# Performance work log

Measured on AMD Instinct MI355X. Metric: run time of the kernel, lower is better.

Reference implementation:

```python
import jax, jax.numpy as jnp
import numpy as np

SCALE, Z, X, Y = 4, 9, 9, 9
INV_SQRT_2PI = 1.0 / np.sqrt(2.0 * np.pi)


def setup_inputs() -> dict:
    key = jax.random.key(0)
    k1, = jax.random.split(key, 1)
    inp = jax.random.normal(k1, (1, 1, 128, 512, 512), dtype=jnp.float32)
    return {
        "inp": inp,
        "mu_z": jnp.asarray(0.0, dtype=jnp.float32),
        "sig_z": jnp.asarray(0.1, dtype=jnp.float32),
        "bet_xy": jnp.asarray(2.0, dtype=jnp.float32),
        "bet_z": jnp.asarray(1.5, dtype=jnp.float32),
    }


def _gen_alf(bet_xy, bet_z):
    # squared distances along each axis; torch's loop overwrites the wrap-around
    # write, so the net result for odd sizes is simply (arange - size//2)**2
    zd = ((jnp.arange(Z) - Z // 2) ** 2).astype(jnp.float32)[:, None, None]
    xd = ((jnp.arange(X) - X // 2) ** 2).astype(jnp.float32)[None, :, None]
    yd = ((jnp.arange(Y) - Y // 2) ** 2).astype(jnp.float32)[None, None, :]
    d_2 = zd / bet_z ** 2 + (xd + yd) / bet_xy ** 2  # (Z, X, Y)
    return jnp.exp(-d_2 / 2) * INV_SQRT_2PI


def reference(inp, mu_z, sig_z, bet_xy, bet_z):
    z0 = jnp.exp(mu_z + 0.5 * sig_z ** 2)
    rec = inp * z0  # (N, 1, D, H, W)
    alf = _gen_alf(bet_xy, bet_z)[None, None]  # (1, 1, Z, X, Y)
    pad_z = (Z - SCALE + 1) // 2
    rec = jax.lax.conv_general_dilated(
        rec, alf,
        window_strides=(SCALE, 1, 1),
        padding=[(pad_z, pad_z), (X // 2, X // 2), (Y // 2, Y // 2)],
        dimension_numbers=("NCDHW", "OIDHW", "NCDHW"),
    )  # (N, 1, D//SCALE, H, W)
    rec = (rec - rec.min()) / (rec.max() - rec.min())
    return rec
```

## Files before the change

kernel.cpp:

```cpp
#include <hip/hip_runtime.h>

#define D_IN  128
#define D_OUT 32
#define H     512
#define W     512
#define W4    128
#define HB    16
#define ZR    (HB + 8)
#define NTHR  512

__global__ __launch_bounds__(NTHR)
void conv3d_fused(const float* __restrict__ inp, float* __restrict__ out,
                  const float* __restrict__ bxy_p, const float* __restrict__ bz_p,
                  float* __restrict__ blkMin, float* __restrict__ blkMax) {
    __shared__ float zbuf[ZR * W];
    __shared__ float hbuf[HB * W];

    const int d  = blockIdx.x >> 5;
    const int h0 = (blockIdx.x & 31) * HB;

    const float bz = bz_p[0], bx = bxy_p[0];
    const float iz = 1.0f / (2.0f * bz * bz);
    const float ix = 1.0f / (2.0f * bx * bx);
    float wz[9], wx[9];
#pragma unroll
    for (int k = 0; k < 9; ++k) {
        float dd = (float)(k - 4);
        wz[k] = expf(-dd * dd * iz);
        wx[k] = expf(-dd * dd * ix);
    }

    const float4* in4 = (const float4*)inp;
    float4* z4 = (float4*)zbuf;
    float4* h4 = (float4*)hbuf;

    for (int t = threadIdx.x; t < ZR * W4; t += NTHR) {
        int r  = t >> 7;
        int c4 = t & (W4 - 1);
        int h  = h0 - 4 + r;
        float4 acc = make_float4(0.f, 0.f, 0.f, 0.f);
        if ((unsigned)h < H) {
            int base = h * W4 + c4;
#pragma unroll
            for (int k = 0; k < 9; ++k) {
                int din = 4 * d - 3 + k;
                if ((unsigned)din < D_IN) {
                    float4 v = in4[din * (H * W4) + base];
                    acc.x += v.x * wz[k]; acc.y += v.y * wz[k];
                    acc.z += v.z * wz[k]; acc.w += v.w * wz[k];
                }
            }
        }
        z4[t] = acc;
    }
    __syncthreads();

    for (int t = threadIdx.x; t < HB * W4; t += NTHR) {
        int r  = t >> 7;
        int c4 = t & (W4 - 1);
        float4 acc = make_float4(0.f, 0.f, 0.f, 0.f);
#pragma unroll
        for (int k = 0; k < 9; ++k) {
            float4 v = z4[(r + k) * W4 + c4];
            acc.x += v.x * wx[k]; acc.y += v.y * wx[k];
            acc.z += v.z * wx[k]; acc.w += v.w * wx[k];
        }
        h4[t] = acc;
    }
    __syncthreads();

    float lmin =  3.402823466e38f;
    float lmax = -3.402823466e38f;
    float4* out4 = (float4*)out;
    for (int t = threadIdx.x; t < HB * W4; t += NTHR) {
        int r  = t >> 7;
        int c4 = t & (W4 - 1);
        float4 zv = make_float4(0.f, 0.f, 0.f, 0.f);
        float4 va = (c4 > 0)      ? h4[r * W4 + c4 - 1] : zv;
        float4 vb =                 h4[r * W4 + c4];
        float4 vc = (c4 < W4 - 1) ? h4[r * W4 + c4 + 1] : zv;
        float win[12] = {va.x, va.y, va.z, va.w,
                         vb.x, vb.y, vb.z, vb.w,
                         vc.x, vc.y, vc.z, vc.w};
        float4 o = make_float4(0.f, 0.f, 0.f, 0.f);
#pragma unroll
        for (int k = 0; k < 9; ++k) {
            o.x += win[k]     * wx[k];
            o.y += win[k + 1] * wx[k];
            o.z += win[k + 2] * wx[k];
            o.w += win[k + 3] * wx[k];
        }
        out4[(d * H + h0 + r) * W4 + c4] = o;
        lmin = fminf(lmin, fminf(fminf(o.x, o.y), fminf(o.z, o.w)));
        lmax = fmaxf(lmax, fmaxf(fmaxf(o.x, o.y), fmaxf(o.z, o.w)));
    }

#pragma unroll
    for (int off = 32; off > 0; off >>= 1) {
        lmin = fminf(lmin, __shfl_down(lmin, off, 64));
        lmax = fmaxf(lmax, __shfl_down(lmax, off, 64));
    }
    float* smin = &zbuf[0];
    float* smax = &zbuf[16];
    int lane = threadIdx.x & 63, wv = threadIdx.x >> 6;
    if (lane == 0) { smin[wv] = lmin; smax[wv] = lmax; }
    __syncthreads();
    if (threadIdx.x == 0) {
        float mn = smin[0], mx = smax[0];
#pragma unroll
        for (int i = 1; i < 8; ++i) { mn = fminf(mn, smin[i]); mx = fmaxf(mx, smax[i]); }
        blkMin[blockIdx.x] = mn;
        blkMax[blockIdx.x] = mx;
    }
}

__global__ void reduce_kernel(const float* __restrict__ blkMin, const float* __restrict__ blkMax,
                              float* __restrict__ fin, int nblk) {
    float lmin =  3.402823466e38f;
    float lmax = -3.402823466e38f;
    for (int i = threadIdx.x; i < nblk; i += blockDim.x) {
        lmin = fminf(lmin, blkMin[i]);
        lmax = fmaxf(lmax, blkMax[i]);
    }
#pragma unroll
    for (int off = 32; off > 0; off >>= 1) {
        lmin = fminf(lmin, __shfl_down(lmin, off, 64));
        lmax = fmaxf(lmax, __shfl_down(lmax, off, 64));
    }
    __shared__ float smin[4], smax[4];
    int lane = threadIdx.x & 63, wv = threadIdx.x >> 6;
    if (lane == 0) { smin[wv] = lmin; smax[wv] = lmax; }
    __syncthreads();
    if (threadIdx.x == 0) {
        fin[0] = fminf(fminf(smin[0], smin[1]), fminf(smin[2], smin[3]));
        fin[1] = fmaxf(fmaxf(smax[0], smax[1]), fmaxf(smax[2], smax[3]));
    }
}

__global__ void norm_kernel(const float* __restrict__ in, float* __restrict__ out,
                            const float* __restrict__ fin) {
    int tid = blockIdx.x * blockDim.x + threadIdx.x;
    float mn  = fin[0];
    float inv = 1.0f / (fin[1] - mn);
    float4 v = ((const float4*)in)[tid];
    ((float4*)out)[tid] = make_float4((v.x - mn) * inv, (v.y - mn) * inv,
                                      (v.z - mn) * inv, (v.w - mn) * inv);
}

extern "C" void kernel_launch(void* const* d_in, const int* in_sizes, int n_in,
                              void* d_out, int out_size, void* d_ws, size_t ws_size,
                              hipStream_t stream) {
    const float* inp    = (const float*)d_in[0];
    const float* bet_xy = (const float*)d_in[3];
    const float* bet_z  = (const float*)d_in[4];
    float* out = (float*)d_out;

    char* ws = (char*)d_ws;
    float* fin    = (float*)ws;
    float* blkMin = (float*)(ws + 4096);
    float* blkMax = (float*)(ws + 8192);
    float* bufA   = (float*)(ws + 65536);

    const int CONV_GRID = D_OUT * (H / HB);
    conv3d_fused<<<CONV_GRID, NTHR, 0, stream>>>(inp, bufA, bet_xy, bet_z, blkMin, blkMax);
    reduce_kernel<<<1, 256, 0, stream>>>(blkMin, blkMax, fin, CONV_GRID);

    const int NTASK = D_OUT * H * W4;
    norm_kernel<<<NTASK / 256, 256, 0, stream>>>(bufA, out, fin);
}
```

Before: 241.4 us.

## Fuse H and W passes via wavefront shuffles, drop intermediate LDS buffer

Merges the H-direction and W-direction conv stages into one loop. Each lane's H-pass result is exchanged with neighbouring lanes through shuffles instead of being written to a shared-memory buffer. Edge lanes (0 and 63) recompute their neighbour's column directly from LDS. This removes the hbuf array (32KB of LDS) and one barrier, which should let more blocks reside per CU; a launch-bounds occupancy hint is added as well. The cost is extra shuffle instructions and divergent redundant work on the two edge lanes.

```diff
diff --git a/kernel.cpp b/kernel.cpp
--- a/kernel.cpp
+++ b/kernel.cpp
@@ -9,12 +9,12 @@
 #define ZR    (HB + 8)
 #define NTHR  512
 
-__global__ __launch_bounds__(NTHR)
+__global__ __launch_bounds__(NTHR, 6)
 void conv3d_fused(const float* __restrict__ inp, float* __restrict__ out,
                   const float* __restrict__ bxy_p, const float* __restrict__ bz_p,
                   float* __restrict__ blkMin, float* __restrict__ blkMax) {
     __shared__ float zbuf[ZR * W];
-    __shared__ float hbuf[HB * W];
+    __shared__ float smin[8], smax[8];
 
     const int d  = blockIdx.x >> 5;
     const int h0 = (blockIdx.x & 31) * HB;
@@ -32,7 +32,6 @@
 
     const float4* in4 = (const float4*)inp;
     float4* z4 = (float4*)zbuf;
-    float4* h4 = (float4*)hbuf;
 
     for (int t = threadIdx.x; t < ZR * W4; t += NTHR) {
         int r  = t >> 7;
@@ -55,32 +54,45 @@
     }
     __syncthreads();
 
+    const int lane = threadIdx.x & 63;
+    float lmin =  3.402823466e38f;
+    float lmax = -3.402823466e38f;
+    float4* out4 = (float4*)out;
+
     for (int t = threadIdx.x; t < HB * W4; t += NTHR) {
         int r  = t >> 7;
         int c4 = t & (W4 - 1);
-        float4 acc = make_float4(0.f, 0.f, 0.f, 0.f);
+
+        float4 v = make_float4(0.f, 0.f, 0.f, 0.f);
 #pragma unroll
         for (int k = 0; k < 9; ++k) {
-            float4 v = z4[(r + k) * W4 + c4];
-            acc.x += v.x * wx[k]; acc.y += v.y * wx[k];
-            acc.z += v.z * wx[k]; acc.w += v.w * wx[k];
+            float4 z = z4[(r + k) * W4 + c4];
+            v.x += z.x * wx[k]; v.y += z.y * wx[k];
+            v.z += z.z * wx[k]; v.w += z.w * wx[k];
         }
-        h4[t] = acc;
-    }
-    __syncthreads();
 
-    float lmin =  3.402823466e38f;
-    float lmax = -3.402823466e38f;
-    float4* out4 = (float4*)out;
-    for (int t = threadIdx.x; t < HB * W4; t += NTHR) {
-        int r  = t >> 7;
-        int c4 = t & (W4 - 1);
-        float4 zv = make_float4(0.f, 0.f, 0.f, 0.f);
-        float4 va = (c4 > 0)      ? h4[r * W4 + c4 - 1] : zv;
-        float4 vb =                 h4[r * W4 + c4];
-        float4 vc = (c4 < W4 - 1) ? h4[r * W4 + c4 + 1] : zv;
+        float4 va, vc;
+        va.x = __shfl_up(v.x, 1, 64);  va.y = __shfl_up(v.y, 1, 64);
+        va.z = __shfl_up(v.z, 1, 64);  va.w = __shfl_up(v.w, 1, 64);
+        vc.x = __shfl_down(v.x, 1, 64); vc.y = __shfl_down(v.y, 1, 64);
+        vc.z = __shfl_down(v.z, 1, 64); vc.w = __shfl_down(v.w, 1, 64);
+
+        if (lane == 0 || lane == 63) {
+            int c4n = c4 + ((lane == 0) ? -1 : 1);
+            float4 vn = make_float4(0.f, 0.f, 0.f, 0.f);
+            if ((unsigned)c4n < W4) {
+#pragma unroll
+                for (int k = 0; k < 9; ++k) {
+                    float4 z = z4[(r + k) * W4 + c4n];
+                    vn.x += z.x * wx[k]; vn.y += z.y * wx[k];
+                    vn.z += z.z * wx[k]; vn.w += z.w * wx[k];
+                }
+            }
+            if (lane == 0) va = vn; else vc = vn;
+        }
+
         float win[12] = {va.x, va.y, va.z, va.w,
-                         vb.x, vb.y, vb.z, vb.w,
+                         v.x,  v.y,  v.z,  v.w,
                          vc.x, vc.y, vc.z, vc.w};
         float4 o = make_float4(0.f, 0.f, 0.f, 0.f);
 #pragma unroll
@@ -100,9 +112,7 @@
         lmin = fminf(lmin, __shfl_down(lmin, off, 64));
         lmax = fmaxf(lmax, __shfl_down(lmax, off, 64));
     }
-    float* smin = &zbuf[0];
-    float* smax = &zbuf[16];
-    int lane = threadIdx.x & 63, wv = threadIdx.x >> 6;
+    int wv = threadIdx.x >> 6;
     if (lane == 0) { smin[wv] = lmin; smax[wv] = lmax; }
     __syncthreads();
     if (threadIdx.x == 0) {
```

Measured after the change: 260.6 us. +8.0%, slower.
